# Performance work log

Measured on AMD Instinct MI355X. Metric: run time of the kernel, lower is better.

The kernel has to match this reference:

```python
import jax, jax.numpy as jnp
import numpy as np

N, E, F, C, ED, G, D = 50000, 1000000, 30, 64, 11, 1024, 256


def setup_inputs() -> dict:
    key = jax.random.key(0)
    ks = jax.random.split(key, 20)
    rn = lambda k, shape, s=0.1: jax.random.normal(k, shape, jnp.float32) * s
    return {
        "x": rn(ks[0], (N, F), 1.0),
        "edge_attr": jax.random.uniform(ks[1], (E, ED), jnp.float32),
        "W0": rn(ks[2], (F, C)), "asrc0": rn(ks[3], (C,)), "adst0": rn(ks[4], (C,)),
        "We0": rn(ks[5], (ED, C)), "ae0": rn(ks[6], (C,)), "Wres0": rn(ks[7], (F, C)),
        "b0": jnp.zeros((C,), jnp.float32),
        "W": rn(ks[8], (3, C, C)), "asrc": rn(ks[9], (3, C)), "adst": rn(ks[10], (3, C)),
        "We": rn(ks[11], (3, ED, C)), "ae": rn(ks[12], (3, C)), "Wres": rn(ks[13], (3, C, C)),
        "b": jnp.zeros((3, C), jnp.float32),
        "Wout": rn(ks[14], (2 * C, D)), "bout": jnp.zeros((D,), jnp.float32),
        "edge_index": jax.random.randint(ks[15], (2, E), 0, N),
        "batch_index": jnp.sort(jax.random.randint(ks[16], (N,), 0, G)),
    }


def _gat(x, src, dst, edge_attr, W, asrc, adst, We, ae, Wres, b):
    """PyG GATConv (heads=1) with edge_dim and residual=True."""
    n = x.shape[0]
    h = x @ W                                   # [N, C]
    e = edge_attr @ We                          # [E, C]
    alpha = (jnp.sum(h * asrc, -1)[src]
             + jnp.sum(h * adst, -1)[dst]
             + jnp.sum(e * ae, -1))             # [E]
    alpha = jax.nn.leaky_relu(alpha, 0.2)
    m = jax.ops.segment_max(alpha, dst, num_segments=n)
    a = jnp.exp(alpha - m[dst])
    s = jax.ops.segment_sum(a, dst, num_segments=n)
    a = a / (s[dst] + 1e-16)                    # per-dst softmax
    out = jax.ops.segment_sum(a[:, None] * h[src], dst, num_segments=n)
    return out + x @ Wres + b


def reference(x, edge_attr, W0, asrc0, adst0, We0, ae0, Wres0, b0,
              W, asrc, adst, We, ae, Wres, b, Wout, bout,
              edge_index, batch_index):
    src, dst = edge_index[0], edge_index[1]
    h = jax.nn.leaky_relu(
        _gat(x, src, dst, edge_attr, W0, asrc0, adst0, We0, ae0, Wres0, b0), 0.01)
    for i in range(3):  # conv1..conv3 (fixed small layer loop)
        h = _gat(h, src, dst, edge_attr, W[i], asrc[i], adst[i],
                 We[i], ae[i], Wres[i], b[i])
        if i < 2:
            h = jax.nn.leaky_relu(h, 0.01)
    gmax = jax.ops.segment_max(h, batch_index, num_segments=G)
    gmax = jnp.where(jnp.isfinite(gmax), gmax, 0.0)  # empty graphs -> 0
    cnt = jax.ops.segment_sum(jnp.ones((h.shape[0],), h.dtype), batch_index,
                              num_segments=G)
    gmean = jax.ops.segment_sum(h, batch_index, num_segments=G) / jnp.maximum(cnt, 1.0)[:, None]
    pooled = jax.nn.leaky_relu(jnp.concatenate([gmax, gmean], axis=1), 0.01)
    return pooled @ Wout + bout
```

## Files before the change

kernel.cpp:

```cpp
#include <hip/hip_runtime.h>
#include <hip/hip_fp16.h>

#define NN 50000
#define NE 1000000
#define FIN0 30
#define C 64
#define ED 11
#define NG 1024
#define DOUT 256
#define NBIN 196
#define PA_EDGES 2048

typedef unsigned long long ull;

__global__ __launch_bounds__(256) void hist196_kernel(const int* __restrict__ dst,
    int* __restrict__ bcnt){
  __shared__ int h[256];
  int t=threadIdx.x;
  h[t]=0;
  __syncthreads();
  for(int i=blockIdx.x*256+t;i<NE;i+=gridDim.x*256)
    atomicAdd(&h[dst[i]>>8],1);
  __syncthreads();
  if(h[t]) atomicAdd(&bcnt[t],h[t]);
}

__global__ __launch_bounds__(256) void scan196_kernel(const int* __restrict__ bcnt,
    int* __restrict__ bbase, int* __restrict__ gcur){
  __shared__ int p[256];
  int t=threadIdx.x;
  int v=bcnt[t];
  p[t]=v; __syncthreads();
  #pragma unroll
  for(int off=1;off<256;off<<=1){
    int u=(t>=off)?p[t-off]:0;
    __syncthreads(); p[t]+=u; __syncthreads();
  }
  int ex=p[t]-v;
  if(t<=NBIN) bbase[t]=ex;
  if(t<NBIN)  gcur[t]=ex;
}

__global__ __launch_bounds__(256) void grow_kernel(const int* __restrict__ batch,
    int* __restrict__ growptr){
  int i=blockIdx.x*256+threadIdx.x;
  if(i>=NN) return;
  int bi=batch[i];
  int bp=(i==0)?-1:batch[i-1];
  for(int g=bp+1;g<=bi;++g) growptr[g]=i;
  if(i==NN-1){ for(int g=bi+1;g<=NG;++g) growptr[g]=NN; }
}

__global__ __launch_bounds__(256) void part_kernel(const int* __restrict__ dst,
    const int* __restrict__ src, const float* __restrict__ edge_attr,
    const float* __restrict__ We0, const float* __restrict__ ae0,
    const float* __restrict__ We,  const float* __restrict__ ae,
    int* __restrict__ gcur,
    ull* __restrict__ pdst_src, float2* __restrict__ ped01, float2* __restrict__ ped23){
  __shared__ ull    ldst_src[PA_EDGES];
  __shared__ float2 led01[PA_EDGES];
  __shared__ float2 led23[PA_EDGES];
  __shared__ unsigned char lbin[PA_EDGES];
  __shared__ float tile[256*ED];
  __shared__ float sw[4][ED];
  __shared__ int hist[256], p[256], sc[256], lofs[256], bb[256];
  int t=threadIdx.x;
  hist[t]=0;
  if(t<4*ED){
    int l=t/ED, j=t%ED;
    const float* wp=(l==0)? (We0+(size_t)j*C) : (We+((size_t)(l-1)*ED+j)*C);
    const float* ap=(l==0)? ae0 : (ae+(size_t)(l-1)*C);
    float s=0.f;
    for(int c=0;c<C;++c) s+=wp[c]*ap[c];
    sw[l][j]=s;
  }
  __syncthreads();
  size_t e0=(size_t)blockIdx.x*PA_EDGES;
  int cnt=(int)min((size_t)PA_EDGES,(size_t)NE-e0);
  for(int i=t;i<cnt;i+=256) atomicAdd(&hist[dst[e0+i]>>8],1);
  __syncthreads();
  p[t]=hist[t]; __syncthreads();
  #pragma unroll
  for(int off=1;off<256;off<<=1){
    int u=(t>=off)?p[t-off]:0;
    __syncthreads(); p[t]+=u; __syncthreads();
  }
  sc[t]=p[t]-hist[t];
  lofs[t]=sc[t];
  bb[t]=(hist[t]>0)?atomicAdd(&gcur[t],hist[t]):0;
  __syncthreads();
  for(int base=0;base<cnt;base+=256){
    int ccnt=min(256,cnt-base);
    for(int i=t;i<ccnt*ED;i+=256) tile[i]=edge_attr[(e0+base)*ED+i];
    __syncthreads();
    if(t<ccnt){
      int i=base+t;
      int d=dst[e0+i], s=src[e0+i];
      int b=d>>8;
      float d0=0,d1=0,d2=0,d3=0;
      #pragma unroll
      for(int j=0;j<ED;++j){
        float ev=tile[t*ED+j];
        d0=fmaf(ev,sw[0][j],d0);
        d1=fmaf(ev,sw[1][j],d1);
        d2=fmaf(ev,sw[2][j],d2);
        d3=fmaf(ev,sw[3][j],d3);
      }
      int slot=atomicAdd(&lofs[b],1);
      ldst_src[slot]=((ull)(unsigned)d<<32)|(unsigned)s;
      led01[slot]=make_float2(d0,d1);
      led23[slot]=make_float2(d2,d3);
      lbin[slot]=(unsigned char)b;
    }
    __syncthreads();
  }
  for(int i=t;i<cnt;i+=256){
    int b=lbin[i];
    int g=bb[b]+i-sc[b];
    pdst_src[g]=ldst_src[i];
    ped01[g]=led01[i];
    ped23[g]=led23[i];
  }
}

__global__ __launch_bounds__(256) void build_kernel(const ull* __restrict__ pdst_src,
    const float2* __restrict__ ped01, const float2* __restrict__ ped23,
    const int* __restrict__ bbase,
    int* __restrict__ rowptr, int* __restrict__ src_csr, float* __restrict__ edc){
  __shared__ int cnt[256], p[256], cur[256];
  int t=threadIdx.x, b=blockIdx.x;
  int n0=b<<8;
  cnt[t]=0;
  __syncthreads();
  int beg=bbase[b], endd=bbase[b+1];
  for(int j=beg+t;j<endd;j+=256)
    atomicAdd(&cnt[(int)(pdst_src[j]>>32)-n0],1);
  __syncthreads();
  int v=cnt[t];
  p[t]=v; __syncthreads();
  #pragma unroll
  for(int off=1;off<256;off<<=1){
    int u=(t>=off)?p[t-off]:0;
    __syncthreads(); p[t]+=u; __syncthreads();
  }
  int ex=p[t]-v;
  cur[t]=beg+ex;
  if(n0+t<NN) rowptr[n0+t]=beg+ex;
  if(b==0&&t==0) rowptr[NN]=NE;
  __syncthreads();
  for(int j=beg+t;j<endd;j+=256){
    ull ds=pdst_src[j];
    int d=(int)(ds>>32);
    int s=(int)(ds&0xffffffffu);
    int pos=atomicAdd(&cur[d-n0],1);
    src_csr[pos]=s;
    float2 a=ped01[j], c=ped23[j];
    edc[pos]=a.x;
    edc[(size_t)NE+pos]=a.y;
    edc[2*(size_t)NE+pos]=c.x;
    edc[3*(size_t)NE+pos]=c.y;
  }
}

template<int FIN, int SXS>
__global__ __launch_bounds__(256) void feat_kernel(const float* __restrict__ in,
    const float* __restrict__ W, const float* __restrict__ Wres,
    const float* __restrict__ bvec, const float* __restrict__ av_src,
    const float* __restrict__ av_dst,
    __half* __restrict__ hW16, float* __restrict__ outb,
    float* __restrict__ as_, float* __restrict__ ad_){
  __shared__ float sW[FIN*C], sR[FIN*C];
  __shared__ float sx[64*SXS];
  __shared__ float sb[C], ss[C], sd[C];
  int tid=threadIdx.x;
  if(tid<C){ sb[tid]=bvec[tid]; ss[tid]=av_src[tid]; sd[tid]=av_dst[tid]; }
  for(int i=tid;i<FIN*C;i+=256){ sW[i]=W[i]; sR[i]=Wres[i]; }
  int nbase=blockIdx.x*64;
  int nvalid=min(64,NN-nbase);
  if constexpr (FIN==64){
    const float4* in4=(const float4*)(in+(size_t)nbase*64);
    for(int i=tid;i<1024;i+=256){
      int n=i>>4, k=(i&15)*4;
      float4 v=(n<nvalid)?in4[i]:make_float4(0.f,0.f,0.f,0.f);
      *(float4*)&sx[n*SXS+k]=v;
    }
  } else {
    for(int i=tid;i<64*FIN;i+=256){
      int n=i/FIN, k=i-n*FIN;
      sx[n*SXS+k]=(n<nvalid)?in[(size_t)(nbase+n)*FIN+k]:0.f;
    }
  }
  __syncthreads();
  int w=tid>>6, lane=tid&63;
  int ng=lane>>4, cl=lane&15;
  int n0=w*16+ng*4;
  int c0=cl*4;
  float hw[4][4]={}, hr[4][4]={};
  const float* sxp=&sx[n0*SXS];
  #pragma unroll 4
  for(int k=0;k<FIN;++k){
    float4 wv=*(const float4*)&sW[k*C+c0];
    float4 rv=*(const float4*)&sR[k*C+c0];
    float xr[4]={sxp[k],sxp[SXS+k],sxp[2*SXS+k],sxp[3*SXS+k]};
    #pragma unroll
    for(int r=0;r<4;++r){
      hw[r][0]=fmaf(xr[r],wv.x,hw[r][0]);
      hw[r][1]=fmaf(xr[r],wv.y,hw[r][1]);
      hw[r][2]=fmaf(xr[r],wv.z,hw[r][2]);
      hw[r][3]=fmaf(xr[r],wv.w,hw[r][3]);
      hr[r][0]=fmaf(xr[r],rv.x,hr[r][0]);
      hr[r][1]=fmaf(xr[r],rv.y,hr[r][1]);
      hr[r][2]=fmaf(xr[r],rv.z,hr[r][2]);
      hr[r][3]=fmaf(xr[r],rv.w,hr[r][3]);
    }
  }
  float s0=ss[c0], s1=ss[c0+1], s2=ss[c0+2], s3=ss[c0+3];
  float d0=sd[c0], d1=sd[c0+1], d2=sd[c0+2], d3=sd[c0+3];
  float b0v=sb[c0], b1v=sb[c0+1], b2v=sb[c0+2], b3v=sb[c0+3];
  #pragma unroll
  for(int r=0;r<4;++r){
    int n=n0+r;
    float ps=hw[r][0]*s0+hw[r][1]*s1+hw[r][2]*s2+hw[r][3]*s3;
    float pd=hw[r][0]*d0+hw[r][1]*d1+hw[r][2]*d2+hw[r][3]*d3;
    #pragma unroll
    for(int off=1;off<16;off<<=1){ ps+=__shfl_xor(ps,off,64); pd+=__shfl_xor(pd,off,64); }
    if(n<nvalid){
      size_t gn=(size_t)(nbase+n);
      ushort4 hv;
      hv.x=__half_as_ushort(__float2half(hw[r][0]));
      hv.y=__half_as_ushort(__float2half(hw[r][1]));
      hv.z=__half_as_ushort(__float2half(hw[r][2]));
      hv.w=__half_as_ushort(__float2half(hw[r][3]));
      *(ushort4*)&hW16[gn*C+c0]=hv;
      float4 ov;
      ov.x=hr[r][0]+b0v; ov.y=hr[r][1]+b1v; ov.z=hr[r][2]+b2v; ov.w=hr[r][3]+b3v;
      *(float4*)&outb[gn*C+c0]=ov;
      if(cl==0){ as_[gn]=ps; ad_[gn]=pd; }
    }
  }
}

__device__ __forceinline__ void acc8(float* a, float at, uint4 u){
  __half2 h0=*(__half2*)&u.x, h1=*(__half2*)&u.y, h2=*(__half2*)&u.z, h3=*(__half2*)&u.w;
  float2 f0=__half22float2(h0), f1=__half22float2(h1);
  float2 f2=__half22float2(h2), f3=__half22float2(h3);
  a[0]=fmaf(at,f0.x,a[0]); a[1]=fmaf(at,f0.y,a[1]);
  a[2]=fmaf(at,f1.x,a[2]); a[3]=fmaf(at,f1.y,a[3]);
  a[4]=fmaf(at,f2.x,a[4]); a[5]=fmaf(at,f2.y,a[5]);
  a[6]=fmaf(at,f3.x,a[6]); a[7]=fmaf(at,f3.y,a[7]);
}

__global__ __launch_bounds__(256) void agg_kernel(const int* __restrict__ rowptr,
    const int* __restrict__ src_csr, const float* __restrict__ edc_l,
    const float* __restrict__ as_, const float* __restrict__ ad_,
    const __half* __restrict__ hW16, float* __restrict__ outb, int relu){
  __shared__ float2 sws[4][64];
  int w=threadIdx.x>>6, lane=threadIdx.x&63;
  int nidx=blockIdx.x*4+w;
  if(nidx>=NN) return;
  int beg=rowptr[nidx], end=rowptr[nidx+1];
  int deg=end-beg;
  float ad_n=ad_[nidx];
  int g2=lane>>3, gl2=lane&7;
  const uint4* hw4=(const uint4*)hW16;
  float s=0.f;
  float acc[8]={0.f,0.f,0.f,0.f,0.f,0.f,0.f,0.f};

  if(deg<=64){
    int j=beg+lane;
    float al=-INFINITY; int sl=0;
    if(lane<deg){
      sl=src_csr[j];
      float a=as_[sl]+ad_n+edc_l[j];
      al=(a>0.f)?a:0.2f*a;
    }
    float mn=al;
    #pragma unroll
    for(int off=32;off;off>>=1) mn=fmaxf(mn,__shfl_xor(mn,off,64));
    float wl=(lane<deg)?__expf(al-mn):0.f;
    s=wl;
    #pragma unroll
    for(int off=32;off;off>>=1) s+=__shfl_xor(s,off,64);
    float2 pr; pr.x=wl; pr.y=__int_as_float(sl);
    sws[w][lane]=pr;
    int t=g2;
    for(; t+8<deg; t+=16){
      float2 r0=sws[w][t], r1=sws[w][t+8];
      uint4 u0=hw4[(size_t)__float_as_int(r0.y)*8+gl2];
      uint4 u1=hw4[(size_t)__float_as_int(r1.y)*8+gl2];
      acc8(acc,r0.x,u0);
      acc8(acc,r1.x,u1);
    }
    if(t<deg){
      float2 r=sws[w][t];
      uint4 u=hw4[(size_t)__float_as_int(r.y)*8+gl2];
      acc8(acc,r.x,u);
    }
  } else {
    float m=-INFINITY;
    for(int base=beg;base<end;base+=64){
      int j=base+lane;
      float al=-INFINITY; int sl=0;
      if(j<end){
        sl=src_csr[j];
        float a=as_[sl]+ad_n+edc_l[j];
        al=(a>0.f)?a:0.2f*a;
      }
      float cm=al;
      #pragma unroll
      for(int off=32;off;off>>=1) cm=fmaxf(cm,__shfl_xor(cm,off,64));
      float mn=fmaxf(m,cm);
      float scale=(m==-INFINITY)?0.f:__expf(m-mn);
      s*=scale;
      #pragma unroll
      for(int i=0;i<8;++i) acc[i]*=scale;
      float wl=(j<end)?__expf(al-mn):0.f;
      float cs=wl;
      #pragma unroll
      for(int off=32;off;off>>=1) cs+=__shfl_xor(cs,off,64);
      s+=cs; m=mn;
      float2 pr; pr.x=wl; pr.y=__int_as_float(sl);
      sws[w][lane]=pr;
      int cnt=min(64,end-base);
      int t=g2;
      for(; t+8<cnt; t+=16){
        float2 r0=sws[w][t], r1=sws[w][t+8];
        uint4 u0=hw4[(size_t)__float_as_int(r0.y)*8+gl2];
        uint4 u1=hw4[(size_t)__float_as_int(r1.y)*8+gl2];
        acc8(acc,r0.x,u0);
        acc8(acc,r1.x,u1);
      }
      if(t<cnt){
        float2 r=sws[w][t];
        uint4 u=hw4[(size_t)__float_as_int(r.y)*8+gl2];
        acc8(acc,r.x,u);
      }
    }
  }

  #pragma unroll
  for(int off=8;off<64;off<<=1){
    #pragma unroll
    for(int i=0;i<8;++i) acc[i]+=__shfl_xor(acc[i],off,64);
  }
  if(g2==0){
    float denom=s+1e-16f;
    size_t o0=(size_t)nidx*C+gl2*8;
    float4 oa=*(float4*)&outb[o0];
    float4 ob=*(float4*)&outb[o0+4];
    float4 va,vb;
    va.x=acc[0]/denom+oa.x; va.y=acc[1]/denom+oa.y;
    va.z=acc[2]/denom+oa.z; va.w=acc[3]/denom+oa.w;
    vb.x=acc[4]/denom+ob.x; vb.y=acc[5]/denom+ob.y;
    vb.z=acc[6]/denom+ob.z; vb.w=acc[7]/denom+ob.w;
    if(relu){
      va.x=(va.x>0.f)?va.x:0.01f*va.x; va.y=(va.y>0.f)?va.y:0.01f*va.y;
      va.z=(va.z>0.f)?va.z:0.01f*va.z; va.w=(va.w>0.f)?va.w:0.01f*va.w;
      vb.x=(vb.x>0.f)?vb.x:0.01f*vb.x; vb.y=(vb.y>0.f)?vb.y:0.01f*vb.y;
      vb.z=(vb.z>0.f)?vb.z:0.01f*vb.z; vb.w=(vb.w>0.f)?vb.w:0.01f*vb.w;
    }
    *(float4*)&outb[o0]=va;
    *(float4*)&outb[o0+4]=vb;
  }
}

__global__ __launch_bounds__(256) void pool_kernel(const float* __restrict__ h,
    const int* __restrict__ growptr, float* __restrict__ pooled){
  int w=threadIdx.x>>6, lane=threadIdx.x&63;
  int g=blockIdx.x*4+w;
  if(g>=NG) return;
  int beg=growptr[g], end=growptr[g+1];
  float mx=-INFINITY, sm=0.f;
  for(int n=beg;n<end;++n){ float v=h[(size_t)n*C+lane]; mx=fmaxf(mx,v); sm+=v; }
  int cnt=end-beg;
  float gm=(cnt==0)?0.f:mx;
  float mean=sm/fmaxf((float)cnt,1.f);
  gm=(gm>0.f)?gm:0.01f*gm;
  mean=(mean>0.f)?mean:0.01f*mean;
  pooled[(size_t)g*128+lane]=gm;
  pooled[(size_t)g*128+64+lane]=mean;
}

__global__ __launch_bounds__(256) void out_kernel(const float* __restrict__ pooled,
    const float* __restrict__ Wout, const float* __restrict__ bout,
    float* __restrict__ out){
  __shared__ float sp[128];
  int g=blockIdx.x, d=threadIdx.x;
  if(d<128) sp[d]=pooled[(size_t)g*128+d];
  __syncthreads();
  float o=bout[d];
  for(int k=0;k<128;++k) o=fmaf(sp[k],Wout[k*DOUT+d],o);
  out[(size_t)g*DOUT+d]=o;
}

extern "C" void kernel_launch(void* const* d_in, const int* in_sizes, int n_in,
                              void* d_out, int out_size, void* d_ws, size_t ws_size,
                              hipStream_t stream){
  const float* x        =(const float*)d_in[0];
  const float* edge_attr=(const float*)d_in[1];
  const float* W0       =(const float*)d_in[2];
  const float* asrc0    =(const float*)d_in[3];
  const float* adst0    =(const float*)d_in[4];
  const float* We0      =(const float*)d_in[5];
  const float* ae0      =(const float*)d_in[6];
  const float* Wres0    =(const float*)d_in[7];
  const float* b0       =(const float*)d_in[8];
  const float* W        =(const float*)d_in[9];
  const float* asrc     =(const float*)d_in[10];
  const float* adst     =(const float*)d_in[11];
  const float* We       =(const float*)d_in[12];
  const float* ae       =(const float*)d_in[13];
  const float* Wres     =(const float*)d_in[14];
  const float* b        =(const float*)d_in[15];
  const float* Wout     =(const float*)d_in[16];
  const float* bout     =(const float*)d_in[17];
  const int* edge_index =(const int*)d_in[18];
  const int* batch_index=(const int*)d_in[19];
  const int* src=edge_index;
  const int* dst=edge_index+NE;

  char* p=(char*)d_ws;
  auto take=[&](size_t bytes)->void*{ void* r=(void*)p; p+=(bytes+255)&~(size_t)255; return r; };
  int* rowptr  =(int*)take((size_t)(NN+1)*4);
  int* growptr =(int*)take((size_t)(NG+1)*4);
  int* bcnt    =(int*)take((size_t)256*4);
  int* bbase   =(int*)take((size_t)256*4);
  int* gcur    =(int*)take((size_t)256*4);
  int* src_csr =(int*)take((size_t)NE*4);
  float* as_   =(float*)take((size_t)NN*4);
  float* ad_   =(float*)take((size_t)NN*4);
  float* edc   =(float*)take((size_t)NE*4*4);
  __half* hW16 =(__half*)take((size_t)NN*C*2);
  float* bufA  =(float*)take((size_t)NN*C*4);
  ull* pdst_src=(ull*)take((size_t)NE*8);
  float* pooled=(float*)pdst_src;
  float2* ped01=(float2*)take((size_t)NE*8);
  float2* ped23=(float2*)take((size_t)NE*8);
  float* bufB  =(float*)ped01;
  (void)ws_size; (void)in_sizes; (void)n_in; (void)out_size;

  hipMemsetAsync(bcnt,0,(size_t)256*4,stream);
  hist196_kernel<<<1024,256,0,stream>>>(dst,bcnt);
  scan196_kernel<<<1,256,0,stream>>>(bcnt,bbase,gcur);
  grow_kernel<<<(NN+255)/256,256,0,stream>>>(batch_index,growptr);

  part_kernel<<<(NE+PA_EDGES-1)/PA_EDGES,256,0,stream>>>(dst,src,edge_attr,
      We0,ae0,We,ae,gcur,pdst_src,ped01,ped23);
  build_kernel<<<NBIN,256,0,stream>>>(pdst_src,ped01,ped23,bbase,rowptr,src_csr,edc);

  const int nblkF=(NN+63)/64;
  const int nblkA=(NN+3)/4;
  feat_kernel<FIN0,36><<<nblkF,256,0,stream>>>(x,W0,Wres0,b0,asrc0,adst0,hW16,bufA,as_,ad_);
  agg_kernel<<<nblkA,256,0,stream>>>(rowptr,src_csr,edc,as_,ad_,hW16,bufA,1);
  float* bin=bufA; float* bo=bufB;
  for(int i=0;i<3;++i){
    feat_kernel<C,68><<<nblkF,256,0,stream>>>(bin,W+(size_t)i*C*C,Wres+(size_t)i*C*C,
        b+(size_t)i*C,asrc+(size_t)i*C,adst+(size_t)i*C,hW16,bo,as_,ad_);
    agg_kernel<<<nblkA,256,0,stream>>>(rowptr,src_csr,edc+(size_t)(i+1)*NE,as_,ad_,hW16,bo,(i<2)?1:0);
    float* t=bin; bin=bo; bo=t;
  }
  pool_kernel<<<(NG+3)/4,256,0,stream>>>(bin,growptr,pooled);
  out_kernel<<<NG,256,0,stream>>>(pooled,Wout,bout,(float*)d_out);
}
```

Baseline: 355.7 us.

## Store per-edge attention terms in fp16, halve partition tile, unroll feat k-loop by two

Per-edge attention contributions (edge_attr·We·ae for four layers) are now stored in half precision, both in the partition staging buffer and in the CSR-ordered arrays. This halves the edge-term traffic in the partition, build and four aggregation passes. The partition tile shrinks from 2048 to 1024 edges per block, and the feature kernel's k-loop is manually unrolled by two using float2 loads of x. The fp16 rounding adds a small error to the attention logits. The ped buffer is now sized from the node arrays and is also reused as bufB.

```diff
diff --git a/kernel.cpp b/kernel.cpp
--- a/kernel.cpp
+++ b/kernel.cpp
@@ -9,7 +9,7 @@
 #define NG 1024
 #define DOUT 256
 #define NBIN 196
-#define PA_EDGES 2048
+#define PA_EDGES 1024
 
 typedef unsigned long long ull;
 
@@ -56,10 +56,9 @@
     const float* __restrict__ We0, const float* __restrict__ ae0,
     const float* __restrict__ We,  const float* __restrict__ ae,
     int* __restrict__ gcur,
-    ull* __restrict__ pdst_src, float2* __restrict__ ped01, float2* __restrict__ ped23){
-  __shared__ ull    ldst_src[PA_EDGES];
-  __shared__ float2 led01[PA_EDGES];
-  __shared__ float2 led23[PA_EDGES];
+    ull* __restrict__ pdst_src, ushort4* __restrict__ ped){
+  __shared__ ull     ldst_src[PA_EDGES];
+  __shared__ ushort4 led[PA_EDGES];
   __shared__ unsigned char lbin[PA_EDGES];
   __shared__ float tile[256*ED];
   __shared__ float sw[4][ED];
@@ -108,8 +107,12 @@
       }
       int slot=atomicAdd(&lofs[b],1);
       ldst_src[slot]=((ull)(unsigned)d<<32)|(unsigned)s;
-      led01[slot]=make_float2(d0,d1);
-      led23[slot]=make_float2(d2,d3);
+      ushort4 hv;
+      hv.x=__half_as_ushort(__float2half(d0));
+      hv.y=__half_as_ushort(__float2half(d1));
+      hv.z=__half_as_ushort(__float2half(d2));
+      hv.w=__half_as_ushort(__float2half(d3));
+      led[slot]=hv;
       lbin[slot]=(unsigned char)b;
     }
     __syncthreads();
@@ -118,15 +121,13 @@
     int b=lbin[i];
     int g=bb[b]+i-sc[b];
     pdst_src[g]=ldst_src[i];
-    ped01[g]=led01[i];
-    ped23[g]=led23[i];
+    ped[g]=led[i];
   }
 }
 
 __global__ __launch_bounds__(256) void build_kernel(const ull* __restrict__ pdst_src,
-    const float2* __restrict__ ped01, const float2* __restrict__ ped23,
-    const int* __restrict__ bbase,
-    int* __restrict__ rowptr, int* __restrict__ src_csr, float* __restrict__ edc){
+    const ushort4* __restrict__ ped, const int* __restrict__ bbase,
+    int* __restrict__ rowptr, int* __restrict__ src_csr, ushort* __restrict__ edch){
   __shared__ int cnt[256], p[256], cur[256];
   int t=threadIdx.x, b=blockIdx.x;
   int n0=b<<8;
@@ -154,11 +155,11 @@
     int s=(int)(ds&0xffffffffu);
     int pos=atomicAdd(&cur[d-n0],1);
     src_csr[pos]=s;
-    float2 a=ped01[j], c=ped23[j];
-    edc[pos]=a.x;
-    edc[(size_t)NE+pos]=a.y;
-    edc[2*(size_t)NE+pos]=c.x;
-    edc[3*(size_t)NE+pos]=c.y;
+    ushort4 e=ped[j];
+    edch[pos]=e.x;
+    edch[(size_t)NE+pos]=e.y;
+    edch[2*(size_t)NE+pos]=e.z;
+    edch[3*(size_t)NE+pos]=e.w;
   }
 }
 
@@ -197,21 +198,36 @@
   int c0=cl*4;
   float hw[4][4]={}, hr[4][4]={};
   const float* sxp=&sx[n0*SXS];
-  #pragma unroll 4
-  for(int k=0;k<FIN;++k){
-    float4 wv=*(const float4*)&sW[k*C+c0];
-    float4 rv=*(const float4*)&sR[k*C+c0];
-    float xr[4]={sxp[k],sxp[SXS+k],sxp[2*SXS+k],sxp[3*SXS+k]};
+  #pragma unroll 2
+  for(int k=0;k<FIN;k+=2){
+    float4 wv0=*(const float4*)&sW[k*C+c0];
+    float4 rv0=*(const float4*)&sR[k*C+c0];
+    float4 wv1=*(const float4*)&sW[(k+1)*C+c0];
+    float4 rv1=*(const float4*)&sR[(k+1)*C+c0];
+    float2 x0=*(const float2*)&sxp[k];
+    float2 x1=*(const float2*)&sxp[SXS+k];
+    float2 x2=*(const float2*)&sxp[2*SXS+k];
+    float2 x3=*(const float2*)&sxp[3*SXS+k];
+    float xa[4]={x0.x,x1.x,x2.x,x3.x};
+    float xb[4]={x0.y,x1.y,x2.y,x3.y};
     #pragma unroll
     for(int r=0;r<4;++r){
-      hw[r][0]=fmaf(xr[r],wv.x,hw[r][0]);
-      hw[r][1]=fmaf(xr[r],wv.y,hw[r][1]);
-      hw[r][2]=fmaf(xr[r],wv.z,hw[r][2]);
-      hw[r][3]=fmaf(xr[r],wv.w,hw[r][3]);
-      hr[r][0]=fmaf(xr[r],rv.x,hr[r][0]);
-      hr[r][1]=fmaf(xr[r],rv.y,hr[r][1]);
-      hr[r][2]=fmaf(xr[r],rv.z,hr[r][2]);
-      hr[r][3]=fmaf(xr[r],rv.w,hr[r][3]);
+      hw[r][0]=fmaf(xa[r],wv0.x,hw[r][0]);
+      hw[r][1]=fmaf(xa[r],wv0.y,hw[r][1]);
+      hw[r][2]=fmaf(xa[r],wv0.z,hw[r][2]);
+      hw[r][3]=fmaf(xa[r],wv0.w,hw[r][3]);
+      hr[r][0]=fmaf(xa[r],rv0.x,hr[r][0]);
+      hr[r][1]=fmaf(xa[r],rv0.y,hr[r][1]);
+      hr[r][2]=fmaf(xa[r],rv0.z,hr[r][2]);
+      hr[r][3]=fmaf(xa[r],rv0.w,hr[r][3]);
+      hw[r][0]=fmaf(xb[r],wv1.x,hw[r][0]);
+      hw[r][1]=fmaf(xb[r],wv1.y,hw[r][1]);
+      hw[r][2]=fmaf(xb[r],wv1.z,hw[r][2]);
+      hw[r][3]=fmaf(xb[r],wv1.w,hw[r][3]);
+      hr[r][0]=fmaf(xb[r],rv1.x,hr[r][0]);
+      hr[r][1]=fmaf(xb[r],rv1.y,hr[r][1]);
+      hr[r][2]=fmaf(xb[r],rv1.z,hr[r][2]);
+      hr[r][3]=fmaf(xb[r],rv1.w,hr[r][3]);
     }
   }
   float s0=ss[c0], s1=ss[c0+1], s2=ss[c0+2], s3=ss[c0+3];
@@ -251,7 +267,7 @@
 }
 
 __global__ __launch_bounds__(256) void agg_kernel(const int* __restrict__ rowptr,
-    const int* __restrict__ src_csr, const float* __restrict__ edc_l,
+    const int* __restrict__ src_csr, const ushort* __restrict__ edc_l,
     const float* __restrict__ as_, const float* __restrict__ ad_,
     const __half* __restrict__ hW16, float* __restrict__ outb, int relu){
   __shared__ float2 sws[4][64];
@@ -271,7 +287,7 @@
     float al=-INFINITY; int sl=0;
     if(lane<deg){
       sl=src_csr[j];
-      float a=as_[sl]+ad_n+edc_l[j];
+      float a=as_[sl]+ad_n+__half2float(__ushort_as_half(edc_l[j]));
       al=(a>0.f)?a:0.2f*a;
     }
     float mn=al;
@@ -303,7 +319,7 @@
       float al=-INFINITY; int sl=0;
       if(j<end){
         sl=src_csr[j];
-        float a=as_[sl]+ad_n+edc_l[j];
+        float a=as_[sl]+ad_n+__half2float(__ushort_as_half(edc_l[j]));
         al=(a>0.f)?a:0.2f*a;
       }
       float cm=al;
@@ -429,14 +445,13 @@
   int* src_csr =(int*)take((size_t)NE*4);
   float* as_   =(float*)take((size_t)NN*4);
   float* ad_   =(float*)take((size_t)NN*4);
-  float* edc   =(float*)take((size_t)NE*4*4);
+  ushort* edch =(ushort*)take((size_t)NE*4*2);
   __half* hW16 =(__half*)take((size_t)NN*C*2);
   float* bufA  =(float*)take((size_t)NN*C*4);
   ull* pdst_src=(ull*)take((size_t)NE*8);
   float* pooled=(float*)pdst_src;
-  float2* ped01=(float2*)take((size_t)NE*8);
-  float2* ped23=(float2*)take((size_t)NE*8);
-  float* bufB  =(float*)ped01;
+  ushort4* ped =(ushort4*)take((size_t)NN*C*4);
+  float* bufB  =(float*)ped;
   (void)ws_size; (void)in_sizes; (void)n_in; (void)out_size;
 
   hipMemsetAsync(bcnt,0,(size_t)256*4,stream);
@@ -445,18 +460,18 @@
   grow_kernel<<<(NN+255)/256,256,0,stream>>>(batch_index,growptr);
 
   part_kernel<<<(NE+PA_EDGES-1)/PA_EDGES,256,0,stream>>>(dst,src,edge_attr,
-      We0,ae0,We,ae,gcur,pdst_src,ped01,ped23);
-  build_kernel<<<NBIN,256,0,stream>>>(pdst_src,ped01,ped23,bbase,rowptr,src_csr,edc);
+      We0,ae0,We,ae,gcur,pdst_src,ped);
+  build_kernel<<<NBIN,256,0,stream>>>(pdst_src,ped,bbase,rowptr,src_csr,edch);
 
   const int nblkF=(NN+63)/64;
   const int nblkA=(NN+3)/4;
   feat_kernel<FIN0,36><<<nblkF,256,0,stream>>>(x,W0,Wres0,b0,asrc0,adst0,hW16,bufA,as_,ad_);
-  agg_kernel<<<nblkA,256,0,stream>>>(rowptr,src_csr,edc,as_,ad_,hW16,bufA,1);
+  agg_kernel<<<nblkA,256,0,stream>>>(rowptr,src_csr,edch,as_,ad_,hW16,bufA,1);
   float* bin=bufA; float* bo=bufB;
   for(int i=0;i<3;++i){
     feat_kernel<C,68><<<nblkF,256,0,stream>>>(bin,W+(size_t)i*C*C,Wres+(size_t)i*C*C,
         b+(size_t)i*C,asrc+(size_t)i*C,adst+(size_t)i*C,hW16,bo,as_,ad_);
-    agg_kernel<<<nblkA,256,0,stream>>>(rowptr,src_csr,edc+(size_t)(i+1)*NE,as_,ad_,hW16,bo,(i<2)?1:0);
+    agg_kernel<<<nblkA,256,0,stream>>>(rowptr,src_csr,edch+(size_t)(i+1)*NE,as_,ad_,hW16,bo,(i<2)?1:0);
     float* t=bin; bin=bo; bo=t;
   }
   pool_kernel<<<(NG+3)/4,256,0,stream>>>(bin,growptr,pooled);
```

New measurement: 338.2 us. 4.9% less time.
